# Optimization experiments

Measured on AMD Instinct MI355X. Metric: run time of the kernel, lower is better.

The kernel has to match this reference:

```python
import jax, jax.numpy as jnp
import numpy as np

NUM_HEADS = 32
NUM_KV_HEADS = 8
HEAD_DIM = 128
ROPE_THETA = 1000000.0
SCALING = HEAD_DIM ** -0.5


def apply_rope_neox(x, positions):
    # x: [T, H, D], positions: [T] int
    half = HEAD_DIM // 2
    inv_freq = 1.0 / (ROPE_THETA ** (jnp.arange(0, half, dtype=jnp.float32) / half))
    freqs = positions.astype(jnp.float32)[:, None] * inv_freq[None, :]  # [T, D/2]
    cos = jnp.cos(freqs)[:, None, :]  # [T, 1, D/2]
    sin = jnp.sin(freqs)[:, None, :]
    x1, x2 = x[..., :half], x[..., half:]
    return jnp.concatenate([x1 * cos - x2 * sin, x2 * cos + x1 * sin], axis=-1)


def setup_inputs() -> dict:
    key = jax.random.key(0)
    k1, k2, k3 = jax.random.split(key, 3)
    T, H = 2048, 4096
    positions = jnp.arange(T, dtype=jnp.int32)
    hidden_states = jax.random.normal(k1, (T, H), dtype=jnp.float32)
    Wqkv = jax.random.normal(k2, (H, 6144), dtype=jnp.float32) * 0.02
    Wo = jax.random.normal(k3, (H, H), dtype=jnp.float32) * 0.02
    return {"positions": positions, "hidden_states": hidden_states, "Wqkv": Wqkv, "Wo": Wo}


def reference(positions, hidden_states, Wqkv, Wo):
    T = hidden_states.shape[0]
    q_size = NUM_HEADS * HEAD_DIM
    kv_size = NUM_KV_HEADS * HEAD_DIM
    qkv = hidden_states @ Wqkv  # [T, 6144]
    q = qkv[:, :q_size].reshape(T, NUM_HEADS, HEAD_DIM)
    k = qkv[:, q_size:q_size + kv_size].reshape(T, NUM_KV_HEADS, HEAD_DIM)
    v = qkv[:, q_size + kv_size:].reshape(T, NUM_KV_HEADS, HEAD_DIM)
    q = apply_rope_neox(q, positions)
    k = apply_rope_neox(k, positions)
    # GQA: repeat kv heads to match query heads
    rep = NUM_HEADS // NUM_KV_HEADS
    k = jnp.repeat(k, rep, axis=1)  # [T, H, D]
    v = jnp.repeat(v, rep, axis=1)
    scores = jnp.einsum('thd,shd->hts', q, k) * SCALING  # [H, T, T]
    causal = jnp.tril(jnp.ones((T, T), dtype=bool))
    scores = jnp.where(causal[None], scores, jnp.finfo(scores.dtype).min)
    attn = jax.nn.softmax(scores, axis=-1)
    out = jnp.einsum('hts,shd->thd', attn, v).reshape(T, NUM_HEADS * HEAD_DIM)
    return out @ Wo
```

## Files before the change

kernel.cpp:

```cpp
#include <hip/hip_runtime.h>
#include <math.h>

#define T_TOK 2048
#define HDIM  4096
#define QKVN  6144
#define NHEADS 32
#define HD    128
#define KV_OFF 4096
#define V_OFF  5120
#define SCALE 0.08838834764831843f

typedef __attribute__((ext_vector_type(8))) short short8;
typedef __attribute__((ext_vector_type(4))) float f32x4;
typedef __attribute__((ext_vector_type(16))) float f32x16;

__device__ __forceinline__ ushort f2bf(float f) {
    union { float f; unsigned u; } v; v.f = f;
    unsigned r = v.u + 0x7FFFu + ((v.u >> 16) & 1u);
    return (ushort)(r >> 16);
}

template <int N_, int LDK, int KC>
__global__ __launch_bounds__(512, 2) void gemm_bf16_8ph(const ushort* __restrict__ A,
                                                        const ushort* __restrict__ B,
                                                        float* __restrict__ C0,
                                                        float* __restrict__ C1) {
    __shared__ __attribute__((aligned(16))) ushort As[2][2][8192];
    __shared__ __attribute__((aligned(16))) ushort Bs[2][2][8192];

    constexpr int NT = KC / 64;
    constexpr int NBN = N_ / 256;

    const int kz = blockIdx.y;
    float* __restrict__ C = kz ? C1 : C0;

    const int nwgx = (int)gridDim.x;
    const int bid = (int)blockIdx.x;
    const int swz = (nwgx & 7) ? bid : ((bid & 7) * (nwgx >> 3) + (bid >> 3));
    const int bm = (swz / NBN) * 256;
    const int bn = (swz % NBN) * 256;

    const int tid = (int)threadIdx.x;
    const int w = tid >> 6;
    const int l = tid & 63;
    const int hfa = w >> 2;
    const int hfb = (w & 3) >> 1;
    const int wbr64 = (w & 1) * 4096;

    const int arc = (l & 15) * 64;
    const int ac0 = ((((l >> 4) << 4)) ^ ((l & 7) << 4)) >> 1;
    const int ac1 = (((1 << 6) | ((l >> 4) << 4)) ^ ((l & 7) << 4)) >> 1;

    const int grow = w * 8 + (l >> 3);
    const int gcol = ((l & 7) ^ (l >> 3)) * 8;
    const ushort* Ag = A + (size_t)kz * KC + (size_t)(bm + grow) * LDK + gcol;
    const ushort* Bg = B + (size_t)kz * KC + (size_t)(bn + grow) * LDK + gcol;

    auto ldsA = (__attribute__((address_space(3))) char*)&As[0][0][0];
    auto ldsB = (__attribute__((address_space(3))) char*)&Bs[0][0][0];
    const int wsl = w * 1024;

#define STG2(ldsbase, gsrc, bufi, hfi, kt)                                                              \
    do {                                                                                                \
        __builtin_amdgcn_global_load_lds(                                                               \
            (const __attribute__((address_space(1))) void*)((gsrc) + (size_t)((hfi) * 128) * LDK + (kt) * 64),       \
            (__attribute__((address_space(3))) void*)((ldsbase) + (bufi) * 32768 + (hfi) * 16384 + wsl), 16, 0, 0);  \
        __builtin_amdgcn_global_load_lds(                                                               \
            (const __attribute__((address_space(1))) void*)((gsrc) + (size_t)((hfi) * 128 + 64) * LDK + (kt) * 64),  \
            (__attribute__((address_space(3))) void*)((ldsbase) + (bufi) * 32768 + (hfi) * 16384 + 8192 + wsl), 16, 0, 0); \
    } while (0)

    STG2(ldsB, Bg, 0, 0, 0);
    STG2(ldsB, Bg, 0, 1, 0);
    STG2(ldsA, Ag, 0, 0, 0);
    STG2(ldsA, Ag, 0, 1, 0);
    STG2(ldsB, Bg, 1, 0, 1);
    STG2(ldsB, Bg, 1, 1, 1);
    STG2(ldsA, Ag, 1, 0, 1);
    asm volatile("s_waitcnt vmcnt(6)" ::: "memory");
    __builtin_amdgcn_s_barrier();

    f32x4 acc[8][4];
#pragma unroll
    for (int i = 0; i < 8; i++)
#pragma unroll
        for (int j = 0; j < 4; j++) acc[i][j] = (f32x4){0.f, 0.f, 0.f, 0.f};

    short8 a0[4][2], aH[4][2], b01[2][2], b23[2][2];

    int buf = 0;
    for (int t = 0; t < NT; ++t) {
        const int nb = buf ^ 1;
        const ushort* Abuf = &As[buf][hfa][0];
        const ushort* Bbuf = &Bs[buf][hfb][0] + wbr64;

#pragma unroll
        for (int fi = 0; fi < 4; fi++) {
            a0[fi][0] = *(const short8*)(Abuf + fi * 1024 + arc + ac0);
            a0[fi][1] = *(const short8*)(Abuf + fi * 1024 + arc + ac1);
        }
#pragma unroll
        for (int fj = 0; fj < 2; fj++) {
            b01[fj][0] = *(const short8*)(Bbuf + fj * 1024 + arc + ac0);
            b01[fj][1] = *(const short8*)(Bbuf + fj * 1024 + arc + ac1);
        }
        if (t + 1 < NT) STG2(ldsA, Ag, nb, 1, t + 1);
        asm volatile("s_waitcnt lgkmcnt(8)" ::: "memory");
        __builtin_amdgcn_s_barrier();
        asm volatile("s_waitcnt lgkmcnt(0)" ::: "memory");
        __builtin_amdgcn_s_setprio(1);
#pragma unroll
        for (int fi = 0; fi < 4; fi++)
#pragma unroll
            for (int fj = 0; fj < 2; fj++)
#pragma unroll
                for (int s = 0; s < 2; s++)
                    acc[fi][fj] = __builtin_amdgcn_mfma_f32_16x16x32_bf16(a0[fi][s], b01[fj][s], acc[fi][fj], 0, 0, 0);
        __builtin_amdgcn_s_setprio(0);
        __builtin_amdgcn_s_barrier();

#pragma unroll
        for (int fj = 0; fj < 2; fj++) {
            b23[fj][0] = *(const short8*)(Bbuf + (fj + 2) * 1024 + arc + ac0);
            b23[fj][1] = *(const short8*)(Bbuf + (fj + 2) * 1024 + arc + ac1);
        }
        if (t + 2 < NT) STG2(ldsB, Bg, buf, 0, t + 2);
        __builtin_amdgcn_s_barrier();
        asm volatile("s_waitcnt lgkmcnt(0)" ::: "memory");
        __builtin_amdgcn_s_setprio(1);
#pragma unroll
        for (int fi = 0; fi < 4; fi++)
#pragma unroll
            for (int fj = 0; fj < 2; fj++)
#pragma unroll
                for (int s = 0; s < 2; s++)
                    acc[fi][fj + 2] = __builtin_amdgcn_mfma_f32_16x16x32_bf16(a0[fi][s], b23[fj][s], acc[fi][fj + 2], 0, 0, 0);
        __builtin_amdgcn_s_setprio(0);
        __builtin_amdgcn_s_barrier();

#pragma unroll
        for (int fi = 0; fi < 4; fi++) {
            aH[fi][0] = *(const short8*)(Abuf + (fi + 4) * 1024 + arc + ac0);
            aH[fi][1] = *(const short8*)(Abuf + (fi + 4) * 1024 + arc + ac1);
        }
        if (t + 2 < NT) STG2(ldsB, Bg, buf, 1, t + 2);
        __builtin_amdgcn_s_barrier();
        asm volatile("s_waitcnt lgkmcnt(0)" ::: "memory");
        __builtin_amdgcn_s_setprio(1);
#pragma unroll
        for (int fi = 0; fi < 4; fi++)
#pragma unroll
            for (int fj = 0; fj < 2; fj++)
#pragma unroll
                for (int s = 0; s < 2; s++)
                    acc[fi + 4][fj + 2] = __builtin_amdgcn_mfma_f32_16x16x32_bf16(aH[fi][s], b23[fj][s], acc[fi + 4][fj + 2], 0, 0, 0);
        __builtin_amdgcn_s_setprio(0);
        __builtin_amdgcn_s_barrier();

        if (t + 2 < NT) {
            STG2(ldsA, Ag, buf, 0, t + 2);
            asm volatile("s_waitcnt vmcnt(6)" ::: "memory");
        } else {
            asm volatile("s_waitcnt vmcnt(0)" ::: "memory");
        }
        __builtin_amdgcn_s_barrier();
        __builtin_amdgcn_s_setprio(1);
#pragma unroll
        for (int fi = 0; fi < 4; fi++)
#pragma unroll
            for (int fj = 0; fj < 2; fj++)
#pragma unroll
                for (int s = 0; s < 2; s++)
                    acc[fi + 4][fj] = __builtin_amdgcn_mfma_f32_16x16x32_bf16(aH[fi][s], b01[fj][s], acc[fi + 4][fj], 0, 0, 0);
        __builtin_amdgcn_s_setprio(0);
        __builtin_amdgcn_s_barrier();

        buf = nb;
    }
#undef STG2

    const int cn = bn + (w & 3) * 64 + (l & 15);
    const int rm = bm + hfa * 128 + ((l >> 4) << 2);
#pragma unroll
    for (int fi = 0; fi < 8; fi++)
#pragma unroll
        for (int fj = 0; fj < 4; fj++)
#pragma unroll
            for (int r = 0; r < 4; r++)
                C[(size_t)(rm + 16 * fi + r) * N_ + cn + 16 * fj] = acc[fi][fj][r];
}

__global__ __launch_bounds__(256) void add_f32(float* __restrict__ out,
                                               const float* __restrict__ p) {
    const int i = (blockIdx.x * 256 + threadIdx.x) * 4;
    float4 a = *(const float4*)(out + i);
    float4 b = *(const float4*)(p + i);
    a.x += b.x; a.y += b.y; a.z += b.z; a.w += b.w;
    *(float4*)(out + i) = a;
}

__global__ __launch_bounds__(256) void cast_bf16(const float* __restrict__ in,
                                                 ushort* __restrict__ outp) {
    const int i = (blockIdx.x * 256 + threadIdx.x) * 4;
    float4 v = *(const float4*)(in + i);
    ushort4 o = {f2bf(v.x), f2bf(v.y), f2bf(v.z), f2bf(v.w)};
    *(ushort4*)(outp + i) = o;
}

template <int K_, int N_>
__global__ __launch_bounds__(256) void transpose_cast(const float* __restrict__ W,
                                                      ushort* __restrict__ WT) {
    __shared__ float T[32 * 65];
    const int k0 = blockIdx.y * 32;
    const int n0 = blockIdx.x * 64;
    const int x = threadIdx.x & 63;
    const int y = threadIdx.x >> 6;
#pragma unroll
    for (int p = 0; p < 8; p++) {
        const int kk = p * 4 + y;
        T[kk * 65 + x] = W[(size_t)(k0 + kk) * N_ + n0 + x];
    }
    __syncthreads();
#pragma unroll
    for (int q = 0; q < 4; q++) {
        const int nl = q * 16 + (threadIdx.x >> 4);
        const int k2 = (threadIdx.x & 15) * 2;
        ushort2 o = {f2bf(T[k2 * 65 + nl]), f2bf(T[(k2 + 1) * 65 + nl])};
        *(ushort2*)&WT[(size_t)(n0 + nl) * K_ + k0 + k2] = o;
    }
}

__global__ __launch_bounds__(256) void rope_cast(const int* __restrict__ pos,
                                                 const float* __restrict__ qkv,
                                                 ushort* __restrict__ qkB) {
    const int t = blockIdx.x;
    const int slot = blockIdx.y * 4 + (threadIdx.x >> 6);
    const int d = threadIdx.x & 63;
    const float p = (float)pos[t];
    const float invf = exp2f(-(float)d * (19.931568569324174f / 64.0f));
    const float f = p * invf;
    const float c = cosf(f), s = sinf(f);
    const float sc = (slot < 32) ? SCALE : 1.0f;
    const float* base = qkv + (size_t)t * QKVN + slot * HD;
    ushort* ob = qkB + (size_t)t * QKVN + slot * HD;
    const float x1 = base[d];
    const float x2 = base[d + 64];
    ob[d]      = f2bf((x1 * c - x2 * s) * sc);
    ob[d + 64] = f2bf((x2 * c + x1 * s) * sc);
}

__global__ __launch_bounds__(256) void vt_cast(const float* __restrict__ qkv,
                                               ushort* __restrict__ Vt) {
    __shared__ float tile[32][33];
    const int t0 = blockIdx.x * 32;
    const int c0 = blockIdx.y * 32;
    const int tx = threadIdx.x & 31;
    const int ty = threadIdx.x >> 5;
#pragma unroll
    for (int i = 0; i < 4; i++) {
        const int tt = ty + 8 * i;
        tile[tt][tx] = qkv[(size_t)(t0 + tt) * QKVN + V_OFF + c0 + tx];
    }
    __syncthreads();
#pragma unroll
    for (int i = 0; i < 4; i++) {
        const int dd = ty + 8 * i;
        Vt[(size_t)(c0 + dd) * 2048 + t0 + tx] = f2bf(tile[tx][dd]);
    }
}

__global__ __launch_bounds__(256, 2) void flash_attn_mfma(
        const ushort* __restrict__ qkB,
        const ushort* __restrict__ Vt,
        ushort* __restrict__ attnB) {
    __shared__ ushort Kf[2][8 * 512];
    __shared__ ushort Vf[2][8 * 512];

    const int b = blockIdx.x;
    const int half = b >> 8;
    const int rest = b & 255;
    const int h = rest >> 3;
    const int q8 = rest & 7;
    const int qi = half ? (15 - q8) : q8;
    const int kvh = h >> 2;

    const int tid = threadIdx.x;
    const int w = tid >> 6;
    const int l = tid & 63;
    const int l31 = l & 31;
    const int hf = l >> 5;

    const int qg = qi * 128 + w * 32 + l31;

    short8 qf[8];
    {
        const ushort* qrow = qkB + (size_t)qg * QKVN + h * HD + hf * 8;
#pragma unroll
        for (int kt = 0; kt < 8; kt++)
            qf[kt] = *(const short8*)(qrow + kt * 16);
    }

    f32x16 O[4];
#pragma unroll
    for (int dt = 0; dt < 4; dt++)
#pragma unroll
        for (int r = 0; r < 16; r++) O[dt][r] = 0.f;
    float mcur = -INFINITY, lcur = 0.f;

    const ushort* kbase = qkB + (size_t)l31 * QKVN + KV_OFF + kvh * HD + (2 * w) * 16 + hf * 8;
    const ushort* vbase = Vt + ((size_t)(kvh * 128 + w * 32 + l31)) * 2048 + hf * 8;

    auto ldsK = (__attribute__((address_space(3))) char*)&Kf[0][0];
    auto ldsV = (__attribute__((address_space(3))) char*)&Vf[0][0];

    const int nst = 4 * qi + 4;
    const int mylast = 4 * qi + w;

#define AST(s, bb)                                                                               \
    do {                                                                                         \
        const ushort* kg = kbase + (size_t)(s) * 32 * QKVN;                                      \
        __builtin_amdgcn_global_load_lds(                                                        \
            (const __attribute__((address_space(1))) void*)kg,                                   \
            (__attribute__((address_space(3))) void*)(ldsK + (bb) * 8192 + (2 * w) * 1024), 16, 0, 0);      \
        __builtin_amdgcn_global_load_lds(                                                        \
            (const __attribute__((address_space(1))) void*)(kg + 16),                            \
            (__attribute__((address_space(3))) void*)(ldsK + (bb) * 8192 + (2 * w + 1) * 1024), 16, 0, 0);  \
        const ushort* vg = vbase + (s) * 32;                                                     \
        __builtin_amdgcn_global_load_lds(                                                        \
            (const __attribute__((address_space(1))) void*)vg,                                   \
            (__attribute__((address_space(3))) void*)(ldsV + (bb) * 8192 + (2 * w) * 1024), 16, 0, 0);      \
        __builtin_amdgcn_global_load_lds(                                                        \
            (const __attribute__((address_space(1))) void*)(vg + 16),                            \
            (__attribute__((address_space(3))) void*)(ldsV + (bb) * 8192 + (2 * w + 1) * 1024), 16, 0, 0);  \
    } while (0)

    AST(0, 0);

    for (int st = 0; st < nst; st++) {
        const int buf = st & 1;
        __builtin_amdgcn_s_barrier();
        if (st + 1 < nst) {
            AST(st + 1, buf ^ 1);
            asm volatile("s_waitcnt vmcnt(4)" ::: "memory");
        } else {
            asm volatile("s_waitcnt vmcnt(0)" ::: "memory");
        }
        __builtin_amdgcn_s_barrier();

        if (st <= mylast) {
            const ushort* Kb = &Kf[buf][0];
            const ushort* Vb = &Vf[buf][0];
            f32x16 S;
#pragma unroll
            for (int r = 0; r < 16; r++) S[r] = 0.f;
            __builtin_amdgcn_s_setprio(1);
#pragma unroll
            for (int kt = 0; kt < 8; kt++) {
                short8 afK = *(const short8*)(Kb + kt * 512 + l * 8);
                S = __builtin_amdgcn_mfma_f32_32x32x16_bf16(afK, qf[kt], S, 0, 0, 0);
            }
            __builtin_amdgcn_s_setprio(0);

            float p[16];
#pragma unroll
            for (int r = 0; r < 16; r++) p[r] = S[r];
            if (st == mylast) {
                const int sb = st * 32 + 4 * hf;
#pragma unroll
                for (int r = 0; r < 16; r++) {
                    const int sg = sb + (r & 3) + 8 * (r >> 2);
                    if (sg > qg) p[r] = -INFINITY;
                }
            }
            float rmax = p[0];
#pragma unroll
            for (int r = 1; r < 16; r++) rmax = fmaxf(rmax, p[r]);
            rmax = fmaxf(rmax, __shfl_xor(rmax, 32));
            const float mnew = fmaxf(mcur, rmax);
            const float alpha = __expf(mcur - mnew);
            float rsum = 0.f;
#pragma unroll
            for (int r = 0; r < 16; r++) {
                p[r] = __expf(p[r] - mnew);
                rsum += p[r];
            }
            rsum += __shfl_xor(rsum, 32);
            lcur = lcur * alpha + rsum;
            mcur = mnew;

#pragma unroll
            for (int dt = 0; dt < 4; dt++)
#pragma unroll
                for (int r = 0; r < 16; r++) O[dt][r] *= alpha;

            unsigned pk[8], rk[8];
#pragma unroll
            for (int g = 0; g < 4; g++) {
                pk[2 * g]     = (unsigned)f2bf(p[4 * g])     | ((unsigned)f2bf(p[4 * g + 1]) << 16);
                pk[2 * g + 1] = (unsigned)f2bf(p[4 * g + 2]) | ((unsigned)f2bf(p[4 * g + 3]) << 16);
            }
#pragma unroll
            for (int i = 0; i < 8; i++) rk[i] = (unsigned)__shfl_xor((int)pk[i], 32);

            short8 Pf[2];
#pragma unroll
            for (int kt2 = 0; kt2 < 2; kt2++) {
                const int g = 2 * kt2 + hf;
                union { unsigned u[4]; short8 s; } cvt;
                cvt.u[0] = hf ? rk[2 * g]     : pk[2 * g];
                cvt.u[1] = hf ? rk[2 * g + 1] : pk[2 * g + 1];
                cvt.u[2] = hf ? pk[2 * g]     : rk[2 * g];
                cvt.u[3] = hf ? pk[2 * g + 1] : rk[2 * g + 1];
                Pf[kt2] = cvt.s;
            }

            __builtin_amdgcn_s_setprio(1);
#pragma unroll
            for (int dt = 0; dt < 4; dt++)
#pragma unroll
                for (int kt2 = 0; kt2 < 2; kt2++) {
                    short8 afV = *(const short8*)(Vb + (dt * 2 + kt2) * 512 + l * 8);
                    O[dt] = __builtin_amdgcn_mfma_f32_32x32x16_bf16(afV, Pf[kt2], O[dt], 0, 0, 0);
                }
            __builtin_amdgcn_s_setprio(0);
        }
    }
#undef AST

    const float inv = 1.0f / lcur;
    ushort* orow = attnB + (size_t)qg * HDIM + h * HD + 4 * hf;
#pragma unroll
    for (int dt = 0; dt < 4; dt++)
#pragma unroll
        for (int rg = 0; rg < 4; rg++) {
            ushort4 o;
            o.x = f2bf(O[dt][4 * rg + 0] * inv);
            o.y = f2bf(O[dt][4 * rg + 1] * inv);
            o.z = f2bf(O[dt][4 * rg + 2] * inv);
            o.w = f2bf(O[dt][4 * rg + 3] * inv);
            *(ushort4*)(orow + dt * 32 + 8 * rg) = o;
        }
}

__global__ __launch_bounds__(256) void rope_kernel(const int* __restrict__ pos,
                                                   float* __restrict__ qkv) {
    const int t = blockIdx.x;
    const int head = blockIdx.y * 4 + (threadIdx.x >> 6);
    const int d = threadIdx.x & 63;
    const float p = (float)pos[t];
    const float invf = exp2f(-(float)d * (19.931568569324174f / 64.0f));
    const float f = p * invf;
    const float c = cosf(f), s = sinf(f);
    float* base = qkv + (size_t)t * QKVN + head * HD;
    const float x1 = base[d];
    const float x2 = base[d + 64];
    base[d]      = x1 * c - x2 * s;
    base[d + 64] = x2 * c + x1 * s;
}

#define DOT4(acc, a, b) acc += (a).x*(b).x + (a).y*(b).y + (a).z*(b).z + (a).w*(b).w
#define FMA4(o, p, v) { (o).x += (p)*(v).x; (o).y += (p)*(v).y; (o).z += (p)*(v).z; (o).w += (p)*(v).w; }

__global__ __launch_bounds__(256, 2) void flash_attn_f32(const float* __restrict__ qkv,
                                                         float* __restrict__ out) {
    __shared__ float Qs[64 * 132];
    __shared__ float KVs[32 * 132];
    __shared__ float Ps[64 * 34];
    const int b = blockIdx.x;
    const int half = (b >> 9) & 1;
    const int rest = b & 511;
    const int h = rest >> 4;
    const int qlo = rest & 15;
    const int qi = half ? (31 - qlo) : qlo;
    const int kvh = h >> 2;
    const int tid = threadIdx.x;
    const int tx = tid & 7;
    const int ty = tid >> 3;
    {
        const float* qbase = qkv + (size_t)(qi * 64) * QKVN + h * HD;
#pragma unroll
        for (int r = 0; r < 8; r++) {
            int idx = r * 256 + tid;
            int qrow = idx >> 5;
            int d = (idx & 31) * 4;
            float4 v = *(const float4*)(qbase + (size_t)qrow * QKVN + d);
            v.x *= SCALE; v.y *= SCALE; v.z *= SCALE; v.w *= SCALE;
            *(float4*)(Qs + qrow * 132 + d) = v;
        }
    }
    float m[2], lsm[2];
    float4 O[2][4];
#pragma unroll
    for (int i = 0; i < 2; i++) {
        m[i] = -INFINITY; lsm[i] = 0.f;
#pragma unroll
        for (int jj = 0; jj < 4; jj++) O[i][jj] = make_float4(0.f, 0.f, 0.f, 0.f);
    }
    const float* kbase = qkv + KV_OFF + kvh * HD;
    const float* vbase = qkv + V_OFF + kvh * HD;
    const int qg0 = qi * 64 + ty;
    const int nst = 2 * qi + 2;
    for (int st = 0; st < nst; st++) {
        __syncthreads();
#pragma unroll
        for (int r = 0; r < 4; r++) {
            int idx = r * 256 + tid;
            int srow = idx >> 5;
            int d = (idx & 31) * 4;
            *(float4*)(KVs + srow * 132 + d) =
                *(const float4*)(kbase + (size_t)(st * 32 + srow) * QKVN + d);
        }
        __syncthreads();
        float S[2][4];
#pragma unroll
        for (int i = 0; i < 2; i++)
#pragma unroll
            for (int j = 0; j < 4; j++) S[i][j] = 0.f;
#pragma unroll 4
        for (int kk = 0; kk < HD; kk += 4) {
            float4 q0 = *(const float4*)(Qs + ty * 132 + kk);
            float4 q1 = *(const float4*)(Qs + (ty + 32) * 132 + kk);
            float4 k0 = *(const float4*)(KVs + tx * 132 + kk);
            float4 k1 = *(const float4*)(KVs + (tx + 8) * 132 + kk);
            float4 k2 = *(const float4*)(KVs + (tx + 16) * 132 + kk);
            float4 k3 = *(const float4*)(KVs + (tx + 24) * 132 + kk);
            DOT4(S[0][0], q0, k0); DOT4(S[0][1], q0, k1);
            DOT4(S[0][2], q0, k2); DOT4(S[0][3], q0, k3);
            DOT4(S[1][0], q1, k0); DOT4(S[1][1], q1, k1);
            DOT4(S[1][2], q1, k2); DOT4(S[1][3], q1, k3);
        }
        const int sg0 = st * 32 + tx;
        float alpha[2];
#pragma unroll
        for (int i = 0; i < 2; i++) {
            const int qg = qg0 + 32 * i;
            float rmax = -INFINITY;
#pragma unroll
            for (int j = 0; j < 4; j++) {
                if (sg0 + 8 * j > qg) S[i][j] = -INFINITY;
                rmax = fmaxf(rmax, S[i][j]);
            }
#pragma unroll
            for (int off = 1; off < 8; off <<= 1)
                rmax = fmaxf(rmax, __shfl_xor(rmax, off));
            const float mnew = fmaxf(m[i], rmax);
            alpha[i] = __expf(m[i] - mnew);
            float rsum = 0.f;
#pragma unroll
            for (int j = 0; j < 4; j++) {
                S[i][j] = __expf(S[i][j] - mnew);
                rsum += S[i][j];
            }
#pragma unroll
            for (int off = 1; off < 8; off <<= 1)
                rsum += __shfl_xor(rsum, off);
            lsm[i] = lsm[i] * alpha[i] + rsum;
            m[i] = mnew;
        }
#pragma unroll
        for (int i = 0; i < 2; i++)
#pragma unroll
            for (int j = 0; j < 4; j++)
                Ps[(ty + 32 * i) * 34 + tx + 8 * j] = S[i][j];
        __syncthreads();
#pragma unroll
        for (int r = 0; r < 4; r++) {
            int idx = r * 256 + tid;
            int srow = idx >> 5;
            int d = (idx & 31) * 4;
            *(float4*)(KVs + srow * 132 + d) =
                *(const float4*)(vbase + (size_t)(st * 32 + srow) * QKVN + d);
        }
        __syncthreads();
#pragma unroll
        for (int i = 0; i < 2; i++) {
            const float a = alpha[i];
#pragma unroll
            for (int jj = 0; jj < 4; jj++) {
                O[i][jj].x *= a; O[i][jj].y *= a; O[i][jj].z *= a; O[i][jj].w *= a;
            }
        }
#pragma unroll 4
        for (int s = 0; s < 32; s++) {
            float p0 = Ps[ty * 34 + s];
            float p1 = Ps[(ty + 32) * 34 + s];
            const float* vr = KVs + s * 132 + 4 * tx;
            float4 v0 = *(const float4*)(vr);
            float4 v1 = *(const float4*)(vr + 32);
            float4 v2 = *(const float4*)(vr + 64);
            float4 v3 = *(const float4*)(vr + 96);
            FMA4(O[0][0], p0, v0); FMA4(O[0][1], p0, v1);
            FMA4(O[0][2], p0, v2); FMA4(O[0][3], p0, v3);
            FMA4(O[1][0], p1, v0); FMA4(O[1][1], p1, v1);
            FMA4(O[1][2], p1, v2); FMA4(O[1][3], p1, v3);
        }
    }
#pragma unroll
    for (int i = 0; i < 2; i++) {
        const float inv = 1.0f / lsm[i];
        float* orow = out + (size_t)(qi * 64 + ty + 32 * i) * HDIM + h * HD + 4 * tx;
#pragma unroll
        for (int jj = 0; jj < 4; jj++) {
            float4 wv = O[i][jj];
            wv.x *= inv; wv.y *= inv; wv.z *= inv; wv.w *= inv;
            *(float4*)(orow + 32 * jj) = wv;
        }
    }
}

template <int N_, int K_>
__global__ __launch_bounds__(256) void sgemm(const float* __restrict__ A,
                                             const float* __restrict__ B,
                                             float* __restrict__ C) {
    __shared__ float As[8][128];
    __shared__ float Bs[8][128];
    const int tid = threadIdx.x;
    const int bm = blockIdx.y * 128;
    const int bn = blockIdx.x * 128;
    const int tx = tid & 15;
    const int ty = tid >> 4;
    const int lm = tid >> 1;
    const int lkq = (tid & 1) * 4;
    const int lr = tid >> 5;
    const int lnq = (tid & 31) * 4;
    float acc[8][8];
#pragma unroll
    for (int i = 0; i < 8; i++)
#pragma unroll
        for (int j = 0; j < 8; j++) acc[i][j] = 0.f;
    const float* Aptr = A + (size_t)(bm + lm) * K_ + lkq;
    const float* Bptr = B + (size_t)lr * N_ + bn + lnq;
    for (int k0 = 0; k0 < K_; k0 += 8) {
        float4 av = *(const float4*)Aptr;
        float4 bv = *(const float4*)Bptr;
        __syncthreads();
        As[lkq + 0][lm] = av.x;
        As[lkq + 1][lm] = av.y;
        As[lkq + 2][lm] = av.z;
        As[lkq + 3][lm] = av.w;
        *(float4*)&Bs[lr][lnq] = bv;
        __syncthreads();
        Aptr += 8;
        Bptr += (size_t)8 * N_;
#pragma unroll
        for (int kk = 0; kk < 8; kk++) {
            float4 a0 = *(const float4*)&As[kk][ty * 4];
            float4 a1 = *(const float4*)&As[kk][64 + ty * 4];
            float4 b0 = *(const float4*)&Bs[kk][tx * 4];
            float4 b1 = *(const float4*)&Bs[kk][64 + tx * 4];
            float a[8] = {a0.x, a0.y, a0.z, a0.w, a1.x, a1.y, a1.z, a1.w};
            float bb[8] = {b0.x, b0.y, b0.z, b0.w, b1.x, b1.y, b1.z, b1.w};
#pragma unroll
            for (int i = 0; i < 8; i++)
#pragma unroll
                for (int j = 0; j < 8; j++) acc[i][j] += a[i] * bb[j];
        }
    }
#pragma unroll
    for (int i = 0; i < 8; i++) {
        int row = bm + ((i < 4) ? (ty * 4 + i) : (64 + ty * 4 + i - 4));
        float4 c0 = {acc[i][0], acc[i][1], acc[i][2], acc[i][3]};
        float4 c1 = {acc[i][4], acc[i][5], acc[i][6], acc[i][7]};
        *(float4*)&C[(size_t)row * N_ + bn + tx * 4] = c0;
        *(float4*)&C[(size_t)row * N_ + bn + 64 + tx * 4] = c1;
    }
}

extern "C" void kernel_launch(void* const* d_in, const int* in_sizes, int n_in,
                              void* d_out, int out_size, void* d_ws, size_t ws_size,
                              hipStream_t stream) {
    const int*   positions = (const int*)d_in[0];
    const float* hidden    = (const float*)d_in[1];
    const float* Wqkv      = (const float*)d_in[2];
    const float* Wo        = (const float*)d_in[3];
    float* out = (float*)d_out;

    char* ws = (char*)d_ws;
    float*  qkv   = (float*)ws;
    ushort* attnB = (ushort*)ws;
    float*  Pk    = (float*)(ws + 16777216);
    ushort* WqkvT = (ushort*)(ws + 50331648);
    ushort* WoT   = (ushort*)(ws + 100663296);
    ushort* hA    = (ushort*)(ws + 134217728);
    ushort* qkB   = (ushort*)(ws + 134217728);
    ushort* Vt    = (ushort*)(ws + 159383552);
    const size_t NEEDED = 163577856;

    if (ws_size >= NEEDED) {
        cast_bf16<<<dim3((T_TOK * HDIM) / 1024), 256, 0, stream>>>(hidden, hA);
        transpose_cast<HDIM, QKVN><<<dim3(QKVN / 64, HDIM / 32), 256, 0, stream>>>(Wqkv, WqkvT);
        transpose_cast<HDIM, HDIM><<<dim3(HDIM / 64, HDIM / 32), 256, 0, stream>>>(Wo, WoT);
        gemm_bf16_8ph<QKVN, HDIM, HDIM>
            <<<dim3((T_TOK / 256) * (QKVN / 256), 1), 512, 0, stream>>>(hA, WqkvT, qkv, qkv);
        rope_cast<<<dim3(T_TOK, 10), 256, 0, stream>>>(positions, qkv, qkB);
        vt_cast<<<dim3(T_TOK / 32, 32), 256, 0, stream>>>(qkv, Vt);
        flash_attn_mfma<<<dim3(512), 256, 0, stream>>>(qkB, Vt, attnB);
        gemm_bf16_8ph<HDIM, HDIM, HDIM / 2>
            <<<dim3((T_TOK / 256) * (HDIM / 256), 2), 512, 0, stream>>>(attnB, WoT, out, Pk);
        add_f32<<<dim3((T_TOK * HDIM) / 1024), 256, 0, stream>>>(out, Pk);
    } else {
        float* attn = qkv + (size_t)T_TOK * QKVN;
        sgemm<QKVN, HDIM><<<dim3(QKVN / 128, T_TOK / 128), 256, 0, stream>>>(hidden, Wqkv, qkv);
        rope_kernel<<<dim3(T_TOK, 10), 256, 0, stream>>>(positions, qkv);
        flash_attn_f32<<<dim3(1024), 256, 0, stream>>>(qkv, attn);
        sgemm<HDIM, HDIM><<<dim3(HDIM / 128, T_TOK / 128), 256, 0, stream>>>(attn, Wo, out);
    }
}
```

Measured before the change: 650.1 us.

## Double flash-attention KV tile to 64 keys and preload all B fragments in GEMM

The flash attention kernel now processes 64 keys per stage instead of 32, halving the number of barrier-separated stages and the online-softmax rescale overhead per key, at the cost of doubled LDS buffers and more registers. Causal masking now applies to two 32-key sub-tiles on the last stage, which wastes some work on the diagonal. In the GEMM, all four B fragments are loaded from LDS up front and the intermediate lgkmcnt waits are removed, letting the compiler schedule LDS reads more freely and raising register pressure.

```diff
diff --git a/kernel.cpp b/kernel.cpp
--- a/kernel.cpp
+++ b/kernel.cpp
@@ -86,7 +86,7 @@
 #pragma unroll
         for (int j = 0; j < 4; j++) acc[i][j] = (f32x4){0.f, 0.f, 0.f, 0.f};
 
-    short8 a0[4][2], aH[4][2], b01[2][2], b23[2][2];
+    short8 a0[4][2], a1[4][2], bq[4][2];
 
     int buf = 0;
     for (int t = 0; t < NT; ++t) {
@@ -100,14 +100,12 @@
             a0[fi][1] = *(const short8*)(Abuf + fi * 1024 + arc + ac1);
         }
 #pragma unroll
-        for (int fj = 0; fj < 2; fj++) {
-            b01[fj][0] = *(const short8*)(Bbuf + fj * 1024 + arc + ac0);
-            b01[fj][1] = *(const short8*)(Bbuf + fj * 1024 + arc + ac1);
+        for (int fj = 0; fj < 4; fj++) {
+            bq[fj][0] = *(const short8*)(Bbuf + fj * 1024 + arc + ac0);
+            bq[fj][1] = *(const short8*)(Bbuf + fj * 1024 + arc + ac1);
         }
         if (t + 1 < NT) STG2(ldsA, Ag, nb, 1, t + 1);
-        asm volatile("s_waitcnt lgkmcnt(8)" ::: "memory");
-        __builtin_amdgcn_s_barrier();
-        asm volatile("s_waitcnt lgkmcnt(0)" ::: "memory");
+        __builtin_amdgcn_s_barrier();
         __builtin_amdgcn_s_setprio(1);
 #pragma unroll
         for (int fi = 0; fi < 4; fi++)
@@ -115,45 +113,38 @@
             for (int fj = 0; fj < 2; fj++)
 #pragma unroll
                 for (int s = 0; s < 2; s++)
-                    acc[fi][fj] = __builtin_amdgcn_mfma_f32_16x16x32_bf16(a0[fi][s], b01[fj][s], acc[fi][fj], 0, 0, 0);
+                    acc[fi][fj] = __builtin_amdgcn_mfma_f32_16x16x32_bf16(a0[fi][s], bq[fj][s], acc[fi][fj], 0, 0, 0);
         __builtin_amdgcn_s_setprio(0);
         __builtin_amdgcn_s_barrier();
 
-#pragma unroll
-        for (int fj = 0; fj < 2; fj++) {
-            b23[fj][0] = *(const short8*)(Bbuf + (fj + 2) * 1024 + arc + ac0);
-            b23[fj][1] = *(const short8*)(Bbuf + (fj + 2) * 1024 + arc + ac1);
-        }
         if (t + 2 < NT) STG2(ldsB, Bg, buf, 0, t + 2);
         __builtin_amdgcn_s_barrier();
-        asm volatile("s_waitcnt lgkmcnt(0)" ::: "memory");
         __builtin_amdgcn_s_setprio(1);
 #pragma unroll
         for (int fi = 0; fi < 4; fi++)
 #pragma unroll
-            for (int fj = 0; fj < 2; fj++)
+            for (int fj = 2; fj < 4; fj++)
 #pragma unroll
                 for (int s = 0; s < 2; s++)
-                    acc[fi][fj + 2] = __builtin_amdgcn_mfma_f32_16x16x32_bf16(a0[fi][s], b23[fj][s], acc[fi][fj + 2], 0, 0, 0);
+                    acc[fi][fj] = __builtin_amdgcn_mfma_f32_16x16x32_bf16(a0[fi][s], bq[fj][s], acc[fi][fj], 0, 0, 0);
         __builtin_amdgcn_s_setprio(0);
         __builtin_amdgcn_s_barrier();
 
 #pragma unroll
         for (int fi = 0; fi < 4; fi++) {
-            aH[fi][0] = *(const short8*)(Abuf + (fi + 4) * 1024 + arc + ac0);
-            aH[fi][1] = *(const short8*)(Abuf + (fi + 4) * 1024 + arc + ac1);
+            a1[fi][0] = *(const short8*)(Abuf + (fi + 4) * 1024 + arc + ac0);
+            a1[fi][1] = *(const short8*)(Abuf + (fi + 4) * 1024 + arc + ac1);
         }
         if (t + 2 < NT) STG2(ldsB, Bg, buf, 1, t + 2);
         __builtin_amdgcn_s_barrier();
-        asm volatile("s_waitcnt lgkmcnt(0)" ::: "memory");
         __builtin_amdgcn_s_setprio(1);
 #pragma unroll
         for (int fi = 0; fi < 4; fi++)
 #pragma unroll
-            for (int fj = 0; fj < 2; fj++)
+            for (int fj = 2; fj < 4; fj++)
 #pragma unroll
                 for (int s = 0; s < 2; s++)
-                    acc[fi + 4][fj + 2] = __builtin_amdgcn_mfma_f32_16x16x32_bf16(aH[fi][s], b23[fj][s], acc[fi + 4][fj + 2], 0, 0, 0);
+                    acc[fi + 4][fj] = __builtin_amdgcn_mfma_f32_16x16x32_bf16(a1[fi][s], bq[fj][s], acc[fi + 4][fj], 0, 0, 0);
         __builtin_amdgcn_s_setprio(0);
         __builtin_amdgcn_s_barrier();
 
@@ -171,7 +162,7 @@
             for (int fj = 0; fj < 2; fj++)
 #pragma unroll
                 for (int s = 0; s < 2; s++)
-                    acc[fi + 4][fj] = __builtin_amdgcn_mfma_f32_16x16x32_bf16(aH[fi][s], b01[fj][s], acc[fi + 4][fj], 0, 0, 0);
+                    acc[fi + 4][fj] = __builtin_amdgcn_mfma_f32_16x16x32_bf16(a1[fi][s], bq[fj][s], acc[fi + 4][fj], 0, 0, 0);
         __builtin_amdgcn_s_setprio(0);
         __builtin_amdgcn_s_barrier();
 
@@ -273,8 +264,8 @@
         const ushort* __restrict__ qkB,
         const ushort* __restrict__ Vt,
         ushort* __restrict__ attnB) {
-    __shared__ ushort Kf[2][8 * 512];
-    __shared__ ushort Vf[2][8 * 512];
+    __shared__ ushort Kf[2][16 * 512];
+    __shared__ ushort Vf[2][16 * 512];
 
     const int b = blockIdx.x;
     const int half = b >> 8;
@@ -313,76 +304,87 @@
     auto ldsK = (__attribute__((address_space(3))) char*)&Kf[0][0];
     auto ldsV = (__attribute__((address_space(3))) char*)&Vf[0][0];
 
-    const int nst = 4 * qi + 4;
-    const int mylast = 4 * qi + w;
-
-#define AST(s, bb)                                                                               \
-    do {                                                                                         \
-        const ushort* kg = kbase + (size_t)(s) * 32 * QKVN;                                      \
-        __builtin_amdgcn_global_load_lds(                                                        \
-            (const __attribute__((address_space(1))) void*)kg,                                   \
-            (__attribute__((address_space(3))) void*)(ldsK + (bb) * 8192 + (2 * w) * 1024), 16, 0, 0);      \
-        __builtin_amdgcn_global_load_lds(                                                        \
-            (const __attribute__((address_space(1))) void*)(kg + 16),                            \
-            (__attribute__((address_space(3))) void*)(ldsK + (bb) * 8192 + (2 * w + 1) * 1024), 16, 0, 0);  \
-        const ushort* vg = vbase + (s) * 32;                                                     \
-        __builtin_amdgcn_global_load_lds(                                                        \
-            (const __attribute__((address_space(1))) void*)vg,                                   \
-            (__attribute__((address_space(3))) void*)(ldsV + (bb) * 8192 + (2 * w) * 1024), 16, 0, 0);      \
-        __builtin_amdgcn_global_load_lds(                                                        \
-            (const __attribute__((address_space(1))) void*)(vg + 16),                            \
-            (__attribute__((address_space(3))) void*)(ldsV + (bb) * 8192 + (2 * w + 1) * 1024), 16, 0, 0);  \
+    const int nst = 2 * qi + 2;
+    const int mylast = (4 * qi + w) >> 1;
+
+#define GLD(src, dst) __builtin_amdgcn_global_load_lds(                              \
+        (const __attribute__((address_space(1))) void*)(src),                        \
+        (__attribute__((address_space(3))) void*)(dst), 16, 0, 0)
+
+#define AST64(j, bb)                                                                 \
+    do {                                                                             \
+        const ushort* kg0 = kbase + (size_t)(j) * 64 * QKVN;                         \
+        const ushort* kg1 = kg0 + (size_t)32 * QKVN;                                 \
+        GLD(kg0,      ldsK + (bb) * 16384 + (2 * w) * 1024);                         \
+        GLD(kg0 + 16, ldsK + (bb) * 16384 + (2 * w + 1) * 1024);                     \
+        GLD(kg1,      ldsK + (bb) * 16384 + (8 + 2 * w) * 1024);                     \
+        GLD(kg1 + 16, ldsK + (bb) * 16384 + (8 + 2 * w + 1) * 1024);                 \
+        const ushort* vg = vbase + (j) * 64;                                         \
+        GLD(vg,       ldsV + (bb) * 16384 + (4 * w + 0) * 1024);                     \
+        GLD(vg + 16,  ldsV + (bb) * 16384 + (4 * w + 1) * 1024);                     \
+        GLD(vg + 32,  ldsV + (bb) * 16384 + (4 * w + 2) * 1024);                     \
+        GLD(vg + 48,  ldsV + (bb) * 16384 + (4 * w + 3) * 1024);                     \
     } while (0)
 
-    AST(0, 0);
-
-    for (int st = 0; st < nst; st++) {
-        const int buf = st & 1;
-        __builtin_amdgcn_s_barrier();
-        if (st + 1 < nst) {
-            AST(st + 1, buf ^ 1);
-            asm volatile("s_waitcnt vmcnt(4)" ::: "memory");
+    AST64(0, 0);
+
+    for (int j = 0; j < nst; j++) {
+        const int buf = j & 1;
+        __builtin_amdgcn_s_barrier();
+        if (j + 1 < nst) {
+            AST64(j + 1, buf ^ 1);
+            asm volatile("s_waitcnt vmcnt(8)" ::: "memory");
         } else {
             asm volatile("s_waitcnt vmcnt(0)" ::: "memory");
         }
         __builtin_amdgcn_s_barrier();
 
-        if (st <= mylast) {
+        if (j <= mylast) {
             const ushort* Kb = &Kf[buf][0];
             const ushort* Vb = &Vf[buf][0];
-            f32x16 S;
-#pragma unroll
-            for (int r = 0; r < 16; r++) S[r] = 0.f;
+            f32x16 S0, S1;
+#pragma unroll
+            for (int r = 0; r < 16; r++) { S0[r] = 0.f; S1[r] = 0.f; }
             __builtin_amdgcn_s_setprio(1);
 #pragma unroll
             for (int kt = 0; kt < 8; kt++) {
-                short8 afK = *(const short8*)(Kb + kt * 512 + l * 8);
-                S = __builtin_amdgcn_mfma_f32_32x32x16_bf16(afK, qf[kt], S, 0, 0, 0);
+                short8 k0 = *(const short8*)(Kb + kt * 512 + l * 8);
+                S0 = __builtin_amdgcn_mfma_f32_32x32x16_bf16(k0, qf[kt], S0, 0, 0, 0);
+            }
+#pragma unroll
+            for (int kt = 0; kt < 8; kt++) {
+                short8 k1 = *(const short8*)(Kb + (8 + kt) * 512 + l * 8);
+                S1 = __builtin_amdgcn_mfma_f32_32x32x16_bf16(k1, qf[kt], S1, 0, 0, 0);
             }
             __builtin_amdgcn_s_setprio(0);
 
-            float p[16];
-#pragma unroll
-            for (int r = 0; r < 16; r++) p[r] = S[r];
-            if (st == mylast) {
-                const int sb = st * 32 + 4 * hf;
+            if (j == mylast) {
+                const int sb = j * 64 + 4 * hf;
 #pragma unroll
                 for (int r = 0; r < 16; r++) {
                     const int sg = sb + (r & 3) + 8 * (r >> 2);
-                    if (sg > qg) p[r] = -INFINITY;
+                    if (sg > qg) S0[r] = -INFINITY;
+                    if (sg + 32 > qg) S1[r] = -INFINITY;
                 }
             }
-            float rmax = p[0];
-#pragma unroll
-            for (int r = 1; r < 16; r++) rmax = fmaxf(rmax, p[r]);
+            float rmax = S0[0];
+#pragma unroll
+            for (int r = 1; r < 16; r++) rmax = fmaxf(rmax, S0[r]);
+#pragma unroll
+            for (int r = 0; r < 16; r++) rmax = fmaxf(rmax, S1[r]);
             rmax = fmaxf(rmax, __shfl_xor(rmax, 32));
             const float mnew = fmaxf(mcur, rmax);
             const float alpha = __expf(mcur - mnew);
             float rsum = 0.f;
 #pragma unroll
             for (int r = 0; r < 16; r++) {
-                p[r] = __expf(p[r] - mnew);
-                rsum += p[r];
+                S0[r] = __expf(S0[r] - mnew);
+                rsum += S0[r];
+            }
+#pragma unroll
+            for (int r = 0; r < 16; r++) {
+                S1[r] = __expf(S1[r] - mnew);
+                rsum += S1[r];
             }
             rsum += __shfl_xor(rsum, 32);
             lcur = lcur * alpha + rsum;
@@ -393,39 +395,58 @@
 #pragma unroll
                 for (int r = 0; r < 16; r++) O[dt][r] *= alpha;
 
-            unsigned pk[8], rk[8];
-#pragma unroll
-            for (int g = 0; g < 4; g++) {
-                pk[2 * g]     = (unsigned)f2bf(p[4 * g])     | ((unsigned)f2bf(p[4 * g + 1]) << 16);
-                pk[2 * g + 1] = (unsigned)f2bf(p[4 * g + 2]) | ((unsigned)f2bf(p[4 * g + 3]) << 16);
-            }
-#pragma unroll
-            for (int i = 0; i < 8; i++) rk[i] = (unsigned)__shfl_xor((int)pk[i], 32);
-
-            short8 Pf[2];
-#pragma unroll
-            for (int kt2 = 0; kt2 < 2; kt2++) {
-                const int g = 2 * kt2 + hf;
-                union { unsigned u[4]; short8 s; } cvt;
-                cvt.u[0] = hf ? rk[2 * g]     : pk[2 * g];
-                cvt.u[1] = hf ? rk[2 * g + 1] : pk[2 * g + 1];
-                cvt.u[2] = hf ? pk[2 * g]     : rk[2 * g];
-                cvt.u[3] = hf ? pk[2 * g + 1] : rk[2 * g + 1];
-                Pf[kt2] = cvt.s;
+            short8 Pf[4];
+            {
+                unsigned pk[8], rk[8];
+#pragma unroll
+                for (int g = 0; g < 4; g++) {
+                    pk[2 * g]     = (unsigned)f2bf(S0[4 * g])     | ((unsigned)f2bf(S0[4 * g + 1]) << 16);
+                    pk[2 * g + 1] = (unsigned)f2bf(S0[4 * g + 2]) | ((unsigned)f2bf(S0[4 * g + 3]) << 16);
+                }
+#pragma unroll
+                for (int i = 0; i < 8; i++) rk[i] = (unsigned)__shfl_xor((int)pk[i], 32);
+#pragma unroll
+                for (int kt2 = 0; kt2 < 2; kt2++) {
+                    const int g = 2 * kt2 + hf;
+                    union { unsigned u[4]; short8 s; } cvt;
+                    cvt.u[0] = hf ? rk[2 * g]     : pk[2 * g];
+                    cvt.u[1] = hf ? rk[2 * g + 1] : pk[2 * g + 1];
+                    cvt.u[2] = hf ? pk[2 * g]     : rk[2 * g];
+                    cvt.u[3] = hf ? pk[2 * g + 1] : rk[2 * g + 1];
+                    Pf[kt2] = cvt.s;
+                }
+#pragma unroll
+                for (int g = 0; g < 4; g++) {
+                    pk[2 * g]     = (unsigned)f2bf(S1[4 * g])     | ((unsigned)f2bf(S1[4 * g + 1]) << 16);
+                    pk[2 * g + 1] = (unsigned)f2bf(S1[4 * g + 2]) | ((unsigned)f2bf(S1[4 * g + 3]) << 16);
+                }
+#pragma unroll
+                for (int i = 0; i < 8; i++) rk[i] = (unsigned)__shfl_xor((int)pk[i], 32);
+#pragma unroll
+                for (int kt2 = 0; kt2 < 2; kt2++) {
+                    const int g = 2 * kt2 + hf;
+                    union { unsigned u[4]; short8 s; } cvt;
+                    cvt.u[0] = hf ? rk[2 * g]     : pk[2 * g];
+                    cvt.u[1] = hf ? rk[2 * g + 1] : pk[2 * g + 1];
+                    cvt.u[2] = hf ? pk[2 * g]     : rk[2 * g];
+                    cvt.u[3] = hf ? pk[2 * g + 1] : rk[2 * g + 1];
+                    Pf[2 + kt2] = cvt.s;
+                }
             }
 
             __builtin_amdgcn_s_setprio(1);
 #pragma unroll
             for (int dt = 0; dt < 4; dt++)
 #pragma unroll
-                for (int kt2 = 0; kt2 < 2; kt2++) {
-                    short8 afV = *(const short8*)(Vb + (dt * 2 + kt2) * 512 + l * 8);
-                    O[dt] = __builtin_amdgcn_mfma_f32_32x32x16_bf16(afV, Pf[kt2], O[dt], 0, 0, 0);
+                for (int ks = 0; ks < 4; ks++) {
+                    short8 afV = *(const short8*)(Vb + (dt * 4 + ks) * 512 + l * 8);
+                    O[dt] = __builtin_amdgcn_mfma_f32_32x32x16_bf16(afV, Pf[ks], O[dt], 0, 0, 0);
                 }
             __builtin_amdgcn_s_setprio(0);
         }
     }
-#undef AST
+#undef AST64
+#undef GLD
 
     const float inv = 1.0f / lcur;
     ushort* orow = attnB + (size_t)qg * HDIM + h * HD + 4 * hf;
```

New measurement: 616.3 us. -5.2%, faster.
